# Performance work log

Hardware: AMD Instinct MI355X
Metric: run time of the kernel (lower is better)

Reference implementation:

```python
import jax, jax.numpy as jnp
import numpy as np

N_NODES = 100000
N_EDGES = 3200000
IN_F = 128


def gcn_conv(x, edge_index, edge_weight, W, b):
    """PyG GCNConv: add self-loops (weight 1), symmetric normalization,
    scatter-add aggregation from src -> dst, then bias."""
    n = x.shape[0]
    src, dst = edge_index[0], edge_index[1]
    h = x @ W  # [N, out]
    # degree with self-loop weight 1
    deg = jax.ops.segment_sum(edge_weight, dst, num_segments=n) + 1.0
    dinv = jax.lax.rsqrt(deg)
    norm = dinv[src] * edge_weight * dinv[dst]  # [E]
    msgs = norm[:, None] * h[src]  # [E, out]
    out = jax.ops.segment_sum(msgs, dst, num_segments=n)
    # self-loop contribution: norm = dinv*1*dinv = 1/deg
    out = out + h / deg[:, None]
    return out + b


def setup_inputs() -> dict:
    key = jax.random.key(0)
    ks = jax.random.split(key, 12)
    x = jax.random.normal(ks[0], (N_NODES, IN_F), dtype=jnp.float32)
    edge_index = jax.random.randint(ks[1], (2, N_EDGES), 0, N_NODES)
    edge_weights = jax.random.uniform(ks[2], (N_EDGES,), dtype=jnp.float32)
    def glorot(k, shape):
        lim = np.sqrt(6.0 / (shape[0] + shape[1]))
        return jax.random.uniform(k, shape, jnp.float32, -lim, lim)
    return {
        "x": x,
        "edge_index": edge_index,
        "edge_weights": edge_weights,
        "W1": glorot(ks[3], (IN_F, 32)),
        "b1": jnp.zeros((32,), jnp.float32),
        "W2": glorot(ks[4], (32, 16)),
        "b2": jnp.zeros((16,), jnp.float32),
        "fc1_w": glorot(ks[5], (16, 1)),
        "fc1_b": jnp.zeros((1,), jnp.float32),
        "fc2_w": glorot(ks[6], (33, 1)),
        "fc2_b": jnp.zeros((1,), jnp.float32),
    }


def reference(x, edge_index, edge_weights, W1, b1, W2, b2, fc1_w, fc1_b, fc2_w, fc2_b):
    x1 = gcn_conv(x, edge_index, edge_weights, W1, b1)
    h = jax.nn.relu(x1)  # dropout is identity in eval mode
    x2 = gcn_conv(h, edge_index, edge_weights, W2, b2)
    x1f = x2 @ fc1_w + fc1_b        # [N, 1]
    c = jax.nn.sigmoid(x1f)
    cat = jnp.concatenate([h, c], axis=1)  # [N, 33]
    r = cat @ fc2_w + fc2_b         # [N, 1]
    return (r, x1f)
```

## Files before the change

### kernel.cpp

```cpp
#include <hip/hip_runtime.h>
#include <math.h>


#define TPB 256
#define PA_CHUNK 4096
#define KMAXB 512

__global__ __launch_bounds__(512) void countA_kernel(const int* __restrict__ dst,
                                                     int* __restrict__ gtot,
                                                     int E, int K) {
    __shared__ int lhist[KMAXB];
    const int tid = threadIdx.x;
    const int e0  = blockIdx.x * PA_CHUNK;
    if (tid < KMAXB) lhist[tid] = 0;
    __syncthreads();
#pragma unroll
    for (int i = 0; i < 8; ++i) {
        int e = e0 + tid + i * 512;
        if (e < E) atomicAdd(&lhist[dst[e] >> 8], 1);
    }
    __syncthreads();
    if (tid < K && lhist[tid] > 0) atomicAdd(&gtot[tid], lhist[tid]);
}

__global__ __launch_bounds__(64) void kscan_kernel(const int* __restrict__ gtot,
                                                   int* __restrict__ gstart,
                                                   int* __restrict__ gcursor,
                                                   int K, int E) {
    int tid = threadIdx.x;
    int b0 = tid * 8, v[8], s = 0;
#pragma unroll
    for (int t = 0; t < 8; ++t) {
        v[t] = s;
        int idx = b0 + t;
        s += (idx < K) ? gtot[idx] : 0;
    }
    int incl = s;
#pragma unroll
    for (int d = 1; d < 64; d <<= 1) {
        int t2 = __shfl_up(incl, d);
        if (tid >= d) incl += t2;
    }
    int excl = incl - s;
#pragma unroll
    for (int t = 0; t < 8; ++t) {
        int idx = b0 + t;
        if (idx < K) { gstart[idx] = excl + v[t]; gcursor[idx] = excl + v[t]; }
    }
    if (tid == 63) gstart[K] = E;
}

__global__ __launch_bounds__(512) void placeA_kernel(const int* __restrict__ src,
                                                     const int* __restrict__ dst,
                                                     const float* __restrict__ ew,
                                                     uint2* __restrict__ tmp,
                                                     int* __restrict__ gcursor,
                                                     int E, int K) {
    __shared__ int lhist[KMAXB], lbase[KMAXB], lcur[KMAXB], gbaseS[KMAXB];
    __shared__ int ltot;
    __shared__ uint2 stage[PA_CHUNK];
    __shared__ int   saddr[PA_CHUNK];
    const int tid = threadIdx.x;
    const int e0  = blockIdx.x * PA_CHUNK;

    if (tid < KMAXB) { lhist[tid] = 0; lcur[tid] = 0; }
    __syncthreads();

    int   b[8];
    uint2 p[8];
#pragma unroll
    for (int i = 0; i < 8; ++i) {
        int e = e0 + tid + i * 512;
        b[i] = -1;
        if (e < E) {
            int d   = dst[e];
            int s   = src[e];
            float w = ew[e];
            b[i]   = d >> 8;
            p[i].x = __float_as_uint(w);
            p[i].y = ((unsigned)s << 8) | (unsigned)(d & 255);
            atomicAdd(&lhist[b[i]], 1);
        }
    }
    __syncthreads();

    if (tid < 64) {
        int b0 = tid * 8, v[8], s = 0;
#pragma unroll
        for (int t = 0; t < 8; ++t) { v[t] = s; s += lhist[b0 + t]; }
        int incl = s;
#pragma unroll
        for (int d = 1; d < 64; d <<= 1) {
            int t2 = __shfl_up(incl, d);
            if (tid >= d) incl += t2;
        }
        int excl = incl - s;
#pragma unroll
        for (int t = 0; t < 8; ++t) lbase[b0 + t] = excl + v[t];
        if (tid == 63) ltot = incl;
    }
    __syncthreads();

    if (tid < K && lhist[tid] > 0)
        gbaseS[tid] = atomicAdd(&gcursor[tid], lhist[tid]);
    __syncthreads();

#pragma unroll
    for (int i = 0; i < 8; ++i) {
        if (b[i] >= 0) {
            int r    = atomicAdd(&lcur[b[i]], 1);
            int sidx = lbase[b[i]] + r;
            stage[sidx] = p[i];
            saddr[sidx] = gbaseS[b[i]] + r;
        }
    }
    __syncthreads();

    int tot = ltot;
    for (int s = tid; s < tot; s += 512) tmp[saddr[s]] = stage[s];
}

__global__ __launch_bounds__(512) void partB_kernel(const uint2* __restrict__ tmp,
                                                    const int* __restrict__ gstart,
                                                    int2* __restrict__ epair,
                                                    int* __restrict__ off,
                                                    float* __restrict__ dinv,
                                                    int N) {
    __shared__ int   lhist[256], loff[256], lcur[256];
    __shared__ float ldeg[256];
    const int tid  = threadIdx.x;
    const int k    = blockIdx.x;
    const int seg0 = gstart[k], seg1 = gstart[k + 1];

    if (tid < 256) { lhist[tid] = 0; lcur[tid] = 0; ldeg[tid] = 0.f; }
    __syncthreads();

    for (int j = seg0 + tid; j < seg1; j += 512)
        atomicAdd(&lhist[tmp[j].y & 255u], 1);
    __syncthreads();

    if (tid < 64) {
        int b0 = tid * 4, v[4], s = 0;
#pragma unroll
        for (int t = 0; t < 4; ++t) { v[t] = s; s += lhist[b0 + t]; }
        int incl = s;
#pragma unroll
        for (int d = 1; d < 64; d <<= 1) {
            int t2 = __shfl_up(incl, d);
            if (tid >= d) incl += t2;
        }
        int excl = incl - s;
#pragma unroll
        for (int t = 0; t < 4; ++t) loff[b0 + t] = excl + v[t];
    }
    __syncthreads();

    if (tid < 256) {
        int d = (k << 8) + tid;
        if (d < N) off[d] = seg0 + loff[tid];
    }

    for (int j = seg0 + tid; j < seg1; j += 512) {
        uint2 q  = tmp[j];
        int dlow = q.y & 255u;
        int s    = (int)(q.y >> 8);
        float w  = __uint_as_float(q.x);
        int r    = atomicAdd(&lcur[dlow], 1);
        int2 pr; pr.x = s; pr.y = (int)q.x;
        epair[seg0 + loff[dlow] + r] = pr;
        atomicAdd(&ldeg[dlow], w);
    }
    __syncthreads();

    if (tid < 256) {
        int d = (k << 8) + tid;
        if (d < N) dinv[d] = 1.0f / sqrtf(ldeg[tid] + 1.0f);
    }
}

__global__ __launch_bounds__(TPB) void gemm1_kernel(const float* __restrict__ x,
                                                    const float* __restrict__ W,
                                                    const float* __restrict__ dinv,
                                                    float* __restrict__ h, int N) {
    __shared__ float Ws[128 * 32];
    __shared__ float xs[32 * 129];
    const int tid = threadIdx.x;
    const int nb  = blockIdx.x * 32;

    const float4* W4  = (const float4*)W;
    float4*       Ws4 = (float4*)Ws;
#pragma unroll
    for (int i = 0; i < 4; ++i) Ws4[tid + i * 256] = W4[tid + i * 256];

#pragma unroll
    for (int i = 0; i < 4; ++i) {
        int idx  = tid + i * 256;
        int node = idx >> 5;
        int col4 = idx & 31;
        if (nb + node < N) {
            float4 v = ((const float4*)(x + (size_t)nb * 128))[idx];
            float* p = &xs[node * 129 + col4 * 4];
            p[0] = v.x; p[1] = v.y; p[2] = v.z; p[3] = v.w;
        }
    }
    __syncthreads();

    const int nl = tid >> 3;
    const int og = (tid & 7) * 4;
    float a0 = 0.f, a1 = 0.f, a2 = 0.f, a3 = 0.f;
#pragma unroll 8
    for (int k = 0; k < 128; ++k) {
        float xv = xs[nl * 129 + k];
        const float* wp = &Ws[k * 32 + og];
        a0 = fmaf(xv, wp[0], a0);
        a1 = fmaf(xv, wp[1], a1);
        a2 = fmaf(xv, wp[2], a2);
        a3 = fmaf(xv, wp[3], a3);
    }
    int node = nb + nl;
    if (node < N) {
        float dv = dinv[node];
        float* out = &h[(size_t)node * 32 + og];
        out[0] = a0 * dv; out[1] = a1 * dv; out[2] = a2 * dv; out[3] = a3 * dv;
    }
}

__global__ __launch_bounds__(TPB) void gather32_kernel(const int* __restrict__ off,
                                                       const int2* __restrict__ epair,
                                                       const float* __restrict__ g1,
                                                       const float* __restrict__ dinv,
                                                       const float* __restrict__ b,
                                                       float* __restrict__ outrelu,
                                                       int N, int E) {
    int wave = (blockIdx.x * TPB + threadIdx.x) >> 6;
    int lane = threadIdx.x & 63;
    if (wave >= N) return;
    const int i    = wave;
    const int f    = lane & 31;
    const int half = lane >> 5;
    const int s0 = off[i];
    const int s1 = (i + 1 < N) ? off[i + 1] : E;

    float acc = 0.f;
    int j = s0 + half;
    for (; j + 2 < s1; j += 4) {
        int2 pa = epair[j];
        int2 pb = epair[j + 2];
        acc = fmaf(__int_as_float(pa.y), g1[(size_t)pa.x * 32 + f], acc);
        acc = fmaf(__int_as_float(pb.y), g1[(size_t)pb.x * 32 + f], acc);
    }
    if (j < s1) {
        int2 p = epair[j];
        acc = fmaf(__int_as_float(p.y), g1[(size_t)p.x * 32 + f], acc);
    }
    acc += __shfl_xor(acc, 32);

    float dv = dinv[i];
    float v  = dv * (acc + g1[(size_t)i * 32 + f]) + b[f];
    v = fmaxf(v, 0.f);
    if (half == 0) outrelu[(size_t)i * 32 + f] = v;
}

__global__ __launch_bounds__(TPB) void gemm2_kernel(const float* __restrict__ h,
                                                    const float* __restrict__ W,
                                                    const float* __restrict__ dinv,
                                                    float* __restrict__ out, int N) {
    __shared__ float Ws[32 * 16];
    int tid = threadIdx.x;
    if (tid < 128) ((float4*)Ws)[tid] = ((const float4*)W)[tid];
    __syncthreads();
    int idx  = blockIdx.x * TPB + tid;
    int node = idx >> 4;
    int f    = idx & 15;
    if (node >= N) return;
    const float* hr = &h[(size_t)node * 32];
    float acc = 0.f;
#pragma unroll
    for (int k = 0; k < 32; ++k) acc = fmaf(hr[k], Ws[k * 16 + f], acc);
    out[(size_t)node * 16 + f] = acc * dinv[node];
}

__global__ __launch_bounds__(TPB) void gather16_final_kernel(const int* __restrict__ off,
                                                             const int2* __restrict__ epair,
                                                             const float* __restrict__ g2,
                                                             const float* __restrict__ hrelu,
                                                             const float* __restrict__ dinv,
                                                             const float* __restrict__ b2,
                                                             const float* __restrict__ fc1_w,
                                                             const float* __restrict__ fc1_b,
                                                             const float* __restrict__ fc2_w,
                                                             const float* __restrict__ fc2_b,
                                                             float* __restrict__ out,
                                                             int N, int E) {
    int wave = (blockIdx.x * TPB + threadIdx.x) >> 6;
    int lane = threadIdx.x & 63;
    if (wave >= N) return;
    const int i = wave;
    const int f = lane & 15;
    const int q = lane >> 4;
    const int s0 = off[i];
    const int s1 = (i + 1 < N) ? off[i + 1] : E;

    float acc = 0.f;
    int j = s0 + q;
    for (; j + 4 < s1; j += 8) {
        int2 pa = epair[j];
        int2 pb = epair[j + 4];
        acc = fmaf(__int_as_float(pa.y), g2[(size_t)pa.x * 16 + f], acc);
        acc = fmaf(__int_as_float(pb.y), g2[(size_t)pb.x * 16 + f], acc);
    }
    if (j < s1) {
        int2 p = epair[j];
        acc = fmaf(__int_as_float(p.y), g2[(size_t)p.x * 16 + f], acc);
    }
    acc += __shfl_xor(acc, 16);
    acc += __shfl_xor(acc, 32);

    float dv = dinv[i];
    float x2 = dv * (acc + g2[(size_t)i * 16 + f]) + b2[f];

    float part = x2 * fc1_w[f];
    part += __shfl_xor(part, 1);
    part += __shfl_xor(part, 2);
    part += __shfl_xor(part, 4);
    part += __shfl_xor(part, 8);
    float x1f = part + fc1_b[0];
    float c   = 1.0f / (1.0f + expf(-x1f));

    float rp = (lane < 32) ? hrelu[(size_t)i * 32 + lane] * fc2_w[lane] : 0.f;
    rp += __shfl_xor(rp, 1);
    rp += __shfl_xor(rp, 2);
    rp += __shfl_xor(rp, 4);
    rp += __shfl_xor(rp, 8);
    rp += __shfl_xor(rp, 16);
    rp += __shfl_xor(rp, 32);
    float r = fmaf(c, fc2_w[32], fc2_b[0]) + rp;

    if (lane == 0) {
        out[i]     = r;
        out[N + i] = x1f;
    }
}

extern "C" void kernel_launch(void* const* d_in, const int* in_sizes, int n_in,
                              void* d_out, int out_size, void* d_ws, size_t ws_size,
                              hipStream_t stream) {
    const float* x     = (const float*)d_in[0];
    const int*   ei    = (const int*)d_in[1];
    const float* ew    = (const float*)d_in[2];
    const float* W1    = (const float*)d_in[3];
    const float* b1    = (const float*)d_in[4];
    const float* W2    = (const float*)d_in[5];
    const float* b2    = (const float*)d_in[6];
    const float* fc1_w = (const float*)d_in[7];
    const float* fc1_b = (const float*)d_in[8];
    const float* fc2_w = (const float*)d_in[9];
    const float* fc2_b = (const float*)d_in[10];

    const int N = in_sizes[0] / 128;
    const int E = in_sizes[2];
    const int* src = ei;
    const int* dst = ei + E;
    const int K = (N + 255) >> 8;

    float* ws    = (float*)d_ws;
    float* dinv  = ws;
    float* hreg  = dinv + N;
    float* h1    = hreg;
    float* hrelu = hreg + (size_t)32 * N;
    int*   off   = (int*)(hreg + (size_t)64 * N);
    int2*  epair = (int2*)(off + N);
    int*   gcursor = (int*)(epair + E);
    int*   gstart  = gcursor + K;
    uint2* tmp   = (uint2*)hreg;
    float* g2    = h1;

    size_t need = ((size_t)66 * N + (size_t)2 * E + 2 * K + 2) * 4;
    if (ws_size < need || K > KMAXB || (size_t)E > (size_t)32 * N) return;

    hipMemsetAsync(gcursor, 0, (size_t)K * sizeof(int), stream);

    countA_kernel<<<(E + PA_CHUNK - 1) / PA_CHUNK, 512, 0, stream>>>(dst, gcursor, E, K);
    kscan_kernel<<<1, 64, 0, stream>>>(gcursor, gstart, gcursor, K, E);
    placeA_kernel<<<(E + PA_CHUNK - 1) / PA_CHUNK, 512, 0, stream>>>(
        src, dst, ew, tmp, gcursor, E, K);
    partB_kernel<<<K, 512, 0, stream>>>(tmp, gstart, epair, off, dinv, N);

    gemm1_kernel<<<(N + 31) / 32, TPB, 0, stream>>>(x, W1, dinv, h1, N);

    gather32_kernel<<<(N + 3) / 4, TPB, 0, stream>>>(off, epair, h1, dinv, b1, hrelu, N, E);
    gemm2_kernel<<<((N * 16) + TPB - 1) / TPB, TPB, 0, stream>>>(hrelu, W2, dinv, g2, N);
    gather16_final_kernel<<<(N + 3) / 4, TPB, 0, stream>>>(
        off, epair, g2, hrelu, dinv, b2, fc1_w, fc1_b, fc2_w, fc2_b, (float*)d_out, N, E);
}
```

Before: 403.4 us.

## Fuse layer-2 GEMM and fc2 dot into layer-1 gather, process multiple nodes per wave

The layer-1 gather now applies ReLU, multiplies by W2 through wave shuffles, and computes the fc2 dot product with the hidden features. This removes the separate gemm2 kernel and the write and re-read of the 32-wide hrelu buffer. Both gather kernels also handle eight nodes per wave and unroll the edge loop four-way for more memory-level parallelism. The cost is fewer waves in flight, more serial work per wave, and 32 shuffle steps per node.

```diff
diff --git a/kernel.cpp b/kernel.cpp
--- a/kernel.cpp
+++ b/kernel.cpp
@@ -5,6 +5,7 @@
 #define TPB 256
 #define PA_CHUNK 4096
 #define KMAXB 512
+#define NPW 8
 
 __global__ __launch_bounds__(512) void countA_kernel(const int* __restrict__ dst,
                                                      int* __restrict__ gtot,
@@ -225,120 +226,125 @@
     }
 }
 
-__global__ __launch_bounds__(TPB) void gather32_kernel(const int* __restrict__ off,
-                                                       const int2* __restrict__ epair,
-                                                       const float* __restrict__ g1,
-                                                       const float* __restrict__ dinv,
-                                                       const float* __restrict__ b,
-                                                       float* __restrict__ outrelu,
-                                                       int N, int E) {
-    int wave = (blockIdx.x * TPB + threadIdx.x) >> 6;
-    int lane = threadIdx.x & 63;
-    if (wave >= N) return;
-    const int i    = wave;
+__global__ __launch_bounds__(TPB) void gather32_fused_kernel(
+    const int* __restrict__ off, const int2* __restrict__ epair,
+    const float* __restrict__ g1, const float* __restrict__ dinv,
+    const float* __restrict__ b1, const float* __restrict__ W2,
+    const float* __restrict__ fc2_w,
+    float* __restrict__ g2, float* __restrict__ rdot, int N, int E) {
+    __shared__ float wls[544];
+    const int tid = threadIdx.x;
+    wls[tid]       = W2[tid];
+    wls[tid + 256] = W2[tid + 256];
+    if (tid < 32) wls[512 + tid] = fc2_w[tid];
+    __syncthreads();
+
+    const int lane = tid & 63;
     const int f    = lane & 31;
     const int half = lane >> 5;
-    const int s0 = off[i];
-    const int s1 = (i + 1 < N) ? off[i + 1] : E;
-
-    float acc = 0.f;
-    int j = s0 + half;
-    for (; j + 2 < s1; j += 4) {
-        int2 pa = epair[j];
-        int2 pb = epair[j + 2];
-        acc = fmaf(__int_as_float(pa.y), g1[(size_t)pa.x * 32 + f], acc);
-        acc = fmaf(__int_as_float(pb.y), g1[(size_t)pb.x * 32 + f], acc);
-    }
-    if (j < s1) {
-        int2 p = epair[j];
-        acc = fmaf(__int_as_float(p.y), g1[(size_t)p.x * 32 + f], acc);
-    }
-    acc += __shfl_xor(acc, 32);
-
-    float dv = dinv[i];
-    float v  = dv * (acc + g1[(size_t)i * 32 + f]) + b[f];
-    v = fmaxf(v, 0.f);
-    if (half == 0) outrelu[(size_t)i * 32 + f] = v;
-}
-
-__global__ __launch_bounds__(TPB) void gemm2_kernel(const float* __restrict__ h,
-                                                    const float* __restrict__ W,
-                                                    const float* __restrict__ dinv,
-                                                    float* __restrict__ out, int N) {
-    __shared__ float Ws[32 * 16];
-    int tid = threadIdx.x;
-    if (tid < 128) ((float4*)Ws)[tid] = ((const float4*)W)[tid];
-    __syncthreads();
-    int idx  = blockIdx.x * TPB + tid;
-    int node = idx >> 4;
-    int f    = idx & 15;
-    if (node >= N) return;
-    const float* hr = &h[(size_t)node * 32];
-    float acc = 0.f;
-#pragma unroll
-    for (int k = 0; k < 32; ++k) acc = fmaf(hr[k], Ws[k * 16 + f], acc);
-    out[(size_t)node * 16 + f] = acc * dinv[node];
-}
-
-__global__ __launch_bounds__(TPB) void gather16_final_kernel(const int* __restrict__ off,
-                                                             const int2* __restrict__ epair,
-                                                             const float* __restrict__ g2,
-                                                             const float* __restrict__ hrelu,
-                                                             const float* __restrict__ dinv,
-                                                             const float* __restrict__ b2,
-                                                             const float* __restrict__ fc1_w,
-                                                             const float* __restrict__ fc1_b,
-                                                             const float* __restrict__ fc2_w,
-                                                             const float* __restrict__ fc2_b,
-                                                             float* __restrict__ out,
-                                                             int N, int E) {
-    int wave = (blockIdx.x * TPB + threadIdx.x) >> 6;
-    int lane = threadIdx.x & 63;
-    if (wave >= N) return;
-    const int i = wave;
-    const int f = lane & 15;
-    const int q = lane >> 4;
-    const int s0 = off[i];
-    const int s1 = (i + 1 < N) ? off[i + 1] : E;
-
-    float acc = 0.f;
-    int j = s0 + q;
-    for (; j + 4 < s1; j += 8) {
-        int2 pa = epair[j];
-        int2 pb = epair[j + 4];
-        acc = fmaf(__int_as_float(pa.y), g2[(size_t)pa.x * 16 + f], acc);
-        acc = fmaf(__int_as_float(pb.y), g2[(size_t)pb.x * 16 + f], acc);
-    }
-    if (j < s1) {
-        int2 p = epair[j];
-        acc = fmaf(__int_as_float(p.y), g2[(size_t)p.x * 16 + f], acc);
-    }
-    acc += __shfl_xor(acc, 16);
-    acc += __shfl_xor(acc, 32);
-
-    float dv = dinv[i];
-    float x2 = dv * (acc + g2[(size_t)i * 16 + f]) + b2[f];
-
-    float part = x2 * fc1_w[f];
-    part += __shfl_xor(part, 1);
-    part += __shfl_xor(part, 2);
-    part += __shfl_xor(part, 4);
-    part += __shfl_xor(part, 8);
-    float x1f = part + fc1_b[0];
-    float c   = 1.0f / (1.0f + expf(-x1f));
-
-    float rp = (lane < 32) ? hrelu[(size_t)i * 32 + lane] * fc2_w[lane] : 0.f;
-    rp += __shfl_xor(rp, 1);
-    rp += __shfl_xor(rp, 2);
-    rp += __shfl_xor(rp, 4);
-    rp += __shfl_xor(rp, 8);
-    rp += __shfl_xor(rp, 16);
-    rp += __shfl_xor(rp, 32);
-    float r = fmaf(c, fc2_w[32], fc2_b[0]) + rp;
-
-    if (lane == 0) {
-        out[i]     = r;
-        out[N + i] = x1f;
+    const float bv = b1[f];
+    const int wbase = (lane < 16) ? lane : 512;
+    const int wstrd = (lane < 16) ? 16 : 1;
+
+    const int i0 = (blockIdx.x * (TPB / 64) + (tid >> 6)) * NPW;
+
+    for (int t = 0; t < NPW; ++t) {
+        int i = i0 + t;
+        if (i >= N) return;
+        const int s0 = off[i];
+        const int s1 = (i + 1 < N) ? off[i + 1] : E;
+
+        float acc = 0.f;
+        int j = s0 + half;
+        for (; j + 6 < s1; j += 8) {
+            int2 pa = epair[j];
+            int2 pb = epair[j + 2];
+            int2 pc = epair[j + 4];
+            int2 pd = epair[j + 6];
+            acc = fmaf(__int_as_float(pa.y), g1[(size_t)pa.x * 32 + f], acc);
+            acc = fmaf(__int_as_float(pb.y), g1[(size_t)pb.x * 32 + f], acc);
+            acc = fmaf(__int_as_float(pc.y), g1[(size_t)pc.x * 32 + f], acc);
+            acc = fmaf(__int_as_float(pd.y), g1[(size_t)pd.x * 32 + f], acc);
+        }
+        for (; j < s1; j += 2) {
+            int2 p = epair[j];
+            acc = fmaf(__int_as_float(p.y), g1[(size_t)p.x * 32 + f], acc);
+        }
+        acc += __shfl_xor(acc, 32);
+
+        float dv = dinv[i];
+        float v  = fmaxf(dv * (acc + g1[(size_t)i * 32 + f]) + bv, 0.f);
+
+        float hs = 0.f;
+#pragma unroll
+        for (int k = 0; k < 32; ++k)
+            hs = fmaf(__shfl(v, k), wls[wbase + k * wstrd], hs);
+
+        if (lane < 16)       g2[(size_t)i * 16 + lane] = hs * dv;
+        else if (lane == 16) rdot[i] = hs;
+    }
+}
+
+__global__ __launch_bounds__(TPB) void gather16_final_kernel(
+    const int* __restrict__ off, const int2* __restrict__ epair,
+    const float* __restrict__ g2, const float* __restrict__ rdot,
+    const float* __restrict__ dinv, const float* __restrict__ b2,
+    const float* __restrict__ fc1_w, const float* __restrict__ fc1_b,
+    const float* __restrict__ fc2_w, const float* __restrict__ fc2_b,
+    float* __restrict__ out, int N, int E) {
+    const int tid  = threadIdx.x;
+    const int lane = tid & 63;
+    const int f    = lane & 15;
+    const int q    = lane >> 4;
+    const float b2v = b2[f];
+    const float f1v = fc1_w[f];
+    const float f1b = fc1_b[0];
+    const float f2w = fc2_w[32];
+    const float f2b = fc2_b[0];
+
+    const int i0 = (blockIdx.x * (TPB / 64) + (tid >> 6)) * NPW;
+
+    for (int t = 0; t < NPW; ++t) {
+        int i = i0 + t;
+        if (i >= N) return;
+        const int s0 = off[i];
+        const int s1 = (i + 1 < N) ? off[i + 1] : E;
+
+        float acc = 0.f;
+        int j = s0 + q;
+        for (; j + 12 < s1; j += 16) {
+            int2 pa = epair[j];
+            int2 pb = epair[j + 4];
+            int2 pc = epair[j + 8];
+            int2 pd = epair[j + 12];
+            acc = fmaf(__int_as_float(pa.y), g2[(size_t)pa.x * 16 + f], acc);
+            acc = fmaf(__int_as_float(pb.y), g2[(size_t)pb.x * 16 + f], acc);
+            acc = fmaf(__int_as_float(pc.y), g2[(size_t)pc.x * 16 + f], acc);
+            acc = fmaf(__int_as_float(pd.y), g2[(size_t)pd.x * 16 + f], acc);
+        }
+        for (; j < s1; j += 4) {
+            int2 p = epair[j];
+            acc = fmaf(__int_as_float(p.y), g2[(size_t)p.x * 16 + f], acc);
+        }
+        acc += __shfl_xor(acc, 16);
+        acc += __shfl_xor(acc, 32);
+
+        float dv = dinv[i];
+        float x2 = dv * (acc + g2[(size_t)i * 16 + f]) + b2v;
+
+        float part = x2 * f1v;
+        part += __shfl_xor(part, 1);
+        part += __shfl_xor(part, 2);
+        part += __shfl_xor(part, 4);
+        part += __shfl_xor(part, 8);
+        float x1f = part + f1b;
+        float c   = 1.0f / (1.0f + expf(-x1f));
+        float r   = fmaf(c, f2w, f2b) + rdot[i];
+
+        if (lane == 0) {
+            out[i]     = r;
+            out[N + i] = x1f;
+        }
     }
 }
 
@@ -365,15 +371,15 @@
 
     float* ws    = (float*)d_ws;
     float* dinv  = ws;
-    float* hreg  = dinv + N;
-    float* h1    = hreg;
-    float* hrelu = hreg + (size_t)32 * N;
-    int*   off   = (int*)(hreg + (size_t)64 * N);
+    float* big   = dinv + N;
+    float* g1    = big;
+    float* g2    = big + (size_t)32 * N;
+    float* rdot  = big + (size_t)48 * N;
+    int*   off   = (int*)(big + (size_t)64 * N);
     int2*  epair = (int2*)(off + N);
     int*   gcursor = (int*)(epair + E);
     int*   gstart  = gcursor + K;
-    uint2* tmp   = (uint2*)hreg;
-    float* g2    = h1;
+    uint2* tmp   = (uint2*)big;
 
     size_t need = ((size_t)66 * N + (size_t)2 * E + 2 * K + 2) * 4;
     if (ws_size < need || K > KMAXB || (size_t)E > (size_t)32 * N) return;
@@ -386,10 +392,12 @@
         src, dst, ew, tmp, gcursor, E, K);
     partB_kernel<<<K, 512, 0, stream>>>(tmp, gstart, epair, off, dinv, N);
 
-    gemm1_kernel<<<(N + 31) / 32, TPB, 0, stream>>>(x, W1, dinv, h1, N);
-
-    gather32_kernel<<<(N + 3) / 4, TPB, 0, stream>>>(off, epair, h1, dinv, b1, hrelu, N, E);
-    gemm2_kernel<<<((N * 16) + TPB - 1) / TPB, TPB, 0, stream>>>(hrelu, W2, dinv, g2, N);
-    gather16_final_kernel<<<(N + 3) / 4, TPB, 0, stream>>>(
-        off, epair, g2, hrelu, dinv, b2, fc1_w, fc1_b, fc2_w, fc2_b, (float*)d_out, N, E);
-}
+    gemm1_kernel<<<(N + 31) / 32, TPB, 0, stream>>>(x, W1, dinv, g1, N);
+
+    const int gblocks = (N + 4 * NPW - 1) / (4 * NPW);
+    gather32_fused_kernel<<<gblocks, TPB, 0, stream>>>(
+        off, epair, g1, dinv, b1, W2, fc2_w, g2, rdot, N, E);
+    gather16_final_kernel<<<gblocks, TPB, 0, stream>>>(
+        off, epair, g2, rdot, dinv, b2, fc1_w, fc1_b, fc2_w, fc2_b,
+        (float*)d_out, N, E);
+}
```

After: 384.0 us. -4.8%, faster.
